# Kernel tuning notes

Measured on AMD Instinct MI355X. Metric: run time of the kernel, lower is better.

## Reference

```python
import jax, jax.numpy as jnp
import numpy as np

_METRIC = (1.0, 1.0, 1.0, 0.0)  # e1,e2,e3 square to +1; e0 (bit 3) squares to 0 (PGA)


def _build_table() -> np.ndarray:
    # Blades ordered by (grade, bits): matches GRADE_INDICES in the source
    # grade1 -> bits 1,2,4,8 at indices 1..4; grade2 -> bits 3,5,6,9,10,12 at 5..10, etc.
    bits_list = sorted(range(16), key=lambda b: (bin(b).count('1'), b))
    idx_of = {b: i for i, b in enumerate(bits_list)}
    table = np.zeros((16, 16, 16), dtype=np.float32)
    for i, bi in enumerate(bits_list):
        for j, bj in enumerate(bits_list):
            swaps = 0
            for k in range(4):
                if (bi >> k) & 1:
                    swaps += bin(bj & ((1 << k) - 1)).count('1')
            coeff = -1.0 if (swaps % 2) else 1.0
            common = bi & bj
            # metric factor: any shared e0 (bit 3) annihilates the term
            if common & 8:
                continue  # metric 0 for e0
            # shared e1/e2/e3 contribute factor +1 (metric +1)
            table[i, j, idx_of[bi ^ bj]] = coeff
    return table


TABLE = jnp.asarray(_build_table())
REV_SIGNS = jnp.asarray(
    [1., 1., 1., 1., 1., -1., -1., -1., -1., -1., -1., -1., -1., -1., -1., 1.],
    dtype=jnp.float32,
)


def geometric_product(a, b):
    # ...i , ...j , ijk -> ...k  (fixed sparse structure-constant contraction)
    return jnp.einsum('...i,...j,ijk->...k', a, b, TABLE.astype(a.dtype))


def setup_inputs() -> dict:
    key = jax.random.key(0)
    kx, km = jax.random.split(key)
    x = jax.random.normal(kx, (16, 262144, 16), dtype=jnp.float32)   # [B, T, 16]
    motor = jax.random.normal(km, (16, 16), dtype=jnp.float32)       # [B, 16]
    return {'x': x, 'motor': motor}


def reference(x, motor):
    # Multivector(x).apply_motor(Multivector(motor)) with 2D motor / 3D data:
    # out = motor * x * reverse(motor), motor broadcast over the token dim.
    signs = REV_SIGNS.astype(motor.dtype)
    m = motor[:, None, :]                # [B, 1, 16] broadcasts over T
    m_rev = (motor * signs)[:, None, :]  # [B, 1, 16]
    tmp = geometric_product(m, x)        # [B, T, 16]
    out = geometric_product(tmp, m_rev)  # [B, T, 16]
    return out
```

## Files before the change

kernel.cpp:

```cpp
#include <hip/hip_runtime.h>

#define PPB 262144
#define NBATCH 16
#define TPB 256
#define NPT 8

typedef float f32x4 __attribute__((ext_vector_type(4)));

static __device__ const int   kBits[16]  = {0,1,2,4,8,3,5,6,9,10,12,7,11,13,14,15};
static __device__ const int   kIdxOf[16] = {0,1,2,5,3,6,7,11,4,8,9,12,10,13,14,15};
static __device__ const float kRev[16]   = {1,1,1,1,1,-1,-1,-1,-1,-1,-1,-1,-1,-1,-1,1};

__global__ void build_sandwich(const float* __restrict__ motor, float* __restrict__ M)
{
    __shared__ float T[16][16][16];
    __shared__ float A[16][16];
    __shared__ float B[16][16];
    __shared__ float m[16], mrev[16];
    const int t = threadIdx.x;
    const int r = t >> 4, c = t & 15;
    const int b = blockIdx.x;

    if (t < 16) { float mv = motor[b * 16 + t]; m[t] = mv; mrev[t] = mv * kRev[t]; }

    #pragma unroll
    for (int k = 0; k < 16; ++k) T[r][c][k] = 0.f;
    {
        const int bi = kBits[r], bj = kBits[c];
        int swaps = 0;
        #pragma unroll
        for (int k = 0; k < 4; ++k)
            if ((bi >> k) & 1) swaps += __popc(bj & ((1 << k) - 1));
        if (!((bi & bj) & 8))
            T[r][c][kIdxOf[bi ^ bj]] = (swaps & 1) ? -1.f : 1.f;
    }
    __syncthreads();

    float av = 0.f, bv = 0.f;
    #pragma unroll
    for (int i = 0; i < 16; ++i) {
        av += m[i]    * T[i][c][r];
        bv += mrev[i] * T[c][i][r];
    }
    A[r][c] = av;
    B[r][c] = bv;
    __syncthreads();

    float acc = 0.f;
    #pragma unroll
    for (int k = 0; k < 16; ++k) acc += B[r][k] * A[k][c];
    M[b * 256 + t] = acc;
}

template<int CTRL>
__device__ inline float dpp1(float v) {
    int i = __float_as_int(v);
    i = __builtin_amdgcn_update_dpp(0, i, CTRL, 0xF, 0xF, true);
    return __int_as_float(i);
}
template<int CTRL>
__device__ inline float4 dpp4(float4 v) {
    float4 r;
    r.x = dpp1<CTRL>(v.x);
    r.y = dpp1<CTRL>(v.y);
    r.z = dpp1<CTRL>(v.z);
    r.w = dpp1<CTRL>(v.w);
    return r;
}

__device__ inline float dot4(float4 a, float4 b) {
    return a.x * b.x + a.y * b.y + a.z * b.z + a.w * b.w;
}

__global__ __launch_bounds__(TPB) void apply_sandwich(
    const f32x4* __restrict__ x, const float* __restrict__ M,
    f32x4* __restrict__ out)
{
    const int t = threadIdx.x;
    const int q = t & 3;
    const int b = blockIdx.y;

    const float* Mb = M + (size_t)b * 256;
    float4 m0_0, m0_1, m0_2, m0_3;
    float4 m1_0, m1_1, m1_2, m1_3;
    float4 m2_0, m2_1, m2_2, m2_3;
    float4 m3_0, m3_1, m3_2, m3_3;
    {
        const int r0 = 4 * q;
        m0_0 = *(const float4*)(Mb + (r0 + 0) * 16 + 4 * (q ^ 0));
        m0_1 = *(const float4*)(Mb + (r0 + 0) * 16 + 4 * (q ^ 1));
        m0_2 = *(const float4*)(Mb + (r0 + 0) * 16 + 4 * (q ^ 2));
        m0_3 = *(const float4*)(Mb + (r0 + 0) * 16 + 4 * (q ^ 3));
        m1_0 = *(const float4*)(Mb + (r0 + 1) * 16 + 4 * (q ^ 0));
        m1_1 = *(const float4*)(Mb + (r0 + 1) * 16 + 4 * (q ^ 1));
        m1_2 = *(const float4*)(Mb + (r0 + 1) * 16 + 4 * (q ^ 2));
        m1_3 = *(const float4*)(Mb + (r0 + 1) * 16 + 4 * (q ^ 3));
        m2_0 = *(const float4*)(Mb + (r0 + 2) * 16 + 4 * (q ^ 0));
        m2_1 = *(const float4*)(Mb + (r0 + 2) * 16 + 4 * (q ^ 1));
        m2_2 = *(const float4*)(Mb + (r0 + 2) * 16 + 4 * (q ^ 2));
        m2_3 = *(const float4*)(Mb + (r0 + 2) * 16 + 4 * (q ^ 3));
        m3_0 = *(const float4*)(Mb + (r0 + 3) * 16 + 4 * (q ^ 0));
        m3_1 = *(const float4*)(Mb + (r0 + 3) * 16 + 4 * (q ^ 1));
        m3_2 = *(const float4*)(Mb + (r0 + 3) * 16 + 4 * (q ^ 2));
        m3_3 = *(const float4*)(Mb + (r0 + 3) * 16 + 4 * (q ^ 3));
    }

    const size_t base = (size_t)b * (PPB * 4) + (size_t)blockIdx.x * (TPB * NPT) + t;

    #pragma unroll
    for (int k = 0; k < NPT; ++k) {
        const size_t g = base + (size_t)k * TPB;
        const f32x4 xv = __builtin_nontemporal_load(&x[g]);
        float4 x0;
        x0.x = xv.x; x0.y = xv.y; x0.z = xv.z; x0.w = xv.w;
        const float4 x1 = dpp4<0xB1>(x0);
        const float4 x2 = dpp4<0x4E>(x0);
        const float4 x3 = dpp4<0x1B>(x0);

        f32x4 acc;
        acc.x = dot4(m0_0, x0) + dot4(m0_1, x1) + dot4(m0_2, x2) + dot4(m0_3, x3);
        acc.y = dot4(m1_0, x0) + dot4(m1_1, x1) + dot4(m1_2, x2) + dot4(m1_3, x3);
        acc.z = dot4(m2_0, x0) + dot4(m2_1, x1) + dot4(m2_2, x2) + dot4(m2_3, x3);
        acc.w = dot4(m3_0, x0) + dot4(m3_1, x1) + dot4(m3_2, x2) + dot4(m3_3, x3);

        __builtin_nontemporal_store(acc, &out[g]);
    }
}

extern "C" void kernel_launch(void* const* d_in, const int* in_sizes, int n_in,
                              void* d_out, int out_size, void* d_ws, size_t ws_size,
                              hipStream_t stream)
{
    const float* x     = (const float*)d_in[0];
    const float* motor = (const float*)d_in[1];
    float* out = (float*)d_out;
    float* M   = (float*)d_ws;

    build_sandwich<<<NBATCH, 256, 0, stream>>>(motor, M);

    dim3 grid(PPB * 4 / (TPB * NPT), NBATCH);
    apply_sandwich<<<grid, TPB, 0, stream>>>((const f32x4*)x, M, (f32x4*)out);
}
```

Before: 96.62 us.

## Fuse sandwich-matrix construction into the apply kernel, dropping the separate launch

Removes the separate build_sandwich kernel and has every block of the main kernel rebuild the 16x16 sandwich matrix for its batch in shared memory. It builds it from the motor with closed-form sign and index lookups packed into 64-bit constants, so no full 16x16x16 structure table is materialised. The intent is to save one kernel launch and the serial dependency between the two kernels. The cost is redundant per-block setup work and three extra barriers before the streaming loop.

```diff
diff --git a/kernel.cpp b/kernel.cpp
--- a/kernel.cpp
+++ b/kernel.cpp
@@ -7,49 +7,19 @@
 
 typedef float f32x4 __attribute__((ext_vector_type(4)));
 
-static __device__ const int   kBits[16]  = {0,1,2,4,8,3,5,6,9,10,12,7,11,13,14,15};
-static __device__ const int   kIdxOf[16] = {0,1,2,5,3,6,7,11,4,8,9,12,10,13,14,15};
-static __device__ const float kRev[16]   = {1,1,1,1,1,-1,-1,-1,-1,-1,-1,-1,-1,-1,-1,1};
+#define PACK_BITS  0xFEDB7CA965384210ull
+#define PACK_IDXOF 0xFEDAC984B7635210ull
+#define REV_NEG_MASK 0x7FE0
 
-__global__ void build_sandwich(const float* __restrict__ motor, float* __restrict__ M)
-{
-    __shared__ float T[16][16][16];
-    __shared__ float A[16][16];
-    __shared__ float B[16][16];
-    __shared__ float m[16], mrev[16];
-    const int t = threadIdx.x;
-    const int r = t >> 4, c = t & 15;
-    const int b = blockIdx.x;
+__device__ __forceinline__ int bits_of(int i) { return (int)((PACK_BITS  >> (4 * i)) & 15ull); }
+__device__ __forceinline__ int idx_of (int b) { return (int)((PACK_IDXOF >> (4 * b)) & 15ull); }
 
-    if (t < 16) { float mv = motor[b * 16 + t]; m[t] = mv; mrev[t] = mv * kRev[t]; }
-
+__device__ __forceinline__ float sign_of(int bl, int br) {
+    int swaps = 0;
     #pragma unroll
-    for (int k = 0; k < 16; ++k) T[r][c][k] = 0.f;
-    {
-        const int bi = kBits[r], bj = kBits[c];
-        int swaps = 0;
-        #pragma unroll
-        for (int k = 0; k < 4; ++k)
-            if ((bi >> k) & 1) swaps += __popc(bj & ((1 << k) - 1));
-        if (!((bi & bj) & 8))
-            T[r][c][kIdxOf[bi ^ bj]] = (swaps & 1) ? -1.f : 1.f;
-    }
-    __syncthreads();
-
-    float av = 0.f, bv = 0.f;
-    #pragma unroll
-    for (int i = 0; i < 16; ++i) {
-        av += m[i]    * T[i][c][r];
-        bv += mrev[i] * T[c][i][r];
-    }
-    A[r][c] = av;
-    B[r][c] = bv;
-    __syncthreads();
-
-    float acc = 0.f;
-    #pragma unroll
-    for (int k = 0; k < 16; ++k) acc += B[r][k] * A[k][c];
-    M[b * 256 + t] = acc;
+    for (int k = 0; k < 4; ++k)
+        if ((bl >> k) & 1) swaps += __popc(br & ((1 << k) - 1));
+    return (swaps & 1) ? -1.f : 1.f;
 }
 
 template<int CTRL>
@@ -72,38 +42,62 @@
     return a.x * b.x + a.y * b.y + a.z * b.z + a.w * b.w;
 }
 
-__global__ __launch_bounds__(TPB) void apply_sandwich(
-    const f32x4* __restrict__ x, const float* __restrict__ M,
+__global__ __launch_bounds__(TPB) void sandwich_fused(
+    const f32x4* __restrict__ x, const float* __restrict__ motor,
     f32x4* __restrict__ out)
 {
+    __shared__ float mS[16], mrevS[16];
+    __shared__ float A[16][16];
+    __shared__ float B[16][16];
+    __shared__ __align__(16) float Ms[16][16];
+
     const int t = threadIdx.x;
     const int q = t & 3;
     const int b = blockIdx.y;
+    const int r = t >> 4, c = t & 15;
 
-    const float* Mb = M + (size_t)b * 256;
-    float4 m0_0, m0_1, m0_2, m0_3;
-    float4 m1_0, m1_1, m1_2, m1_3;
-    float4 m2_0, m2_1, m2_2, m2_3;
-    float4 m3_0, m3_1, m3_2, m3_3;
+    if (t < 16) {
+        float mv = motor[b * 16 + t];
+        mS[t] = mv;
+        mrevS[t] = ((REV_NEG_MASK >> t) & 1) ? -mv : mv;
+    }
+    __syncthreads();
+
     {
-        const int r0 = 4 * q;
-        m0_0 = *(const float4*)(Mb + (r0 + 0) * 16 + 4 * (q ^ 0));
-        m0_1 = *(const float4*)(Mb + (r0 + 0) * 16 + 4 * (q ^ 1));
-        m0_2 = *(const float4*)(Mb + (r0 + 0) * 16 + 4 * (q ^ 2));
-        m0_3 = *(const float4*)(Mb + (r0 + 0) * 16 + 4 * (q ^ 3));
-        m1_0 = *(const float4*)(Mb + (r0 + 1) * 16 + 4 * (q ^ 0));
-        m1_1 = *(const float4*)(Mb + (r0 + 1) * 16 + 4 * (q ^ 1));
-        m1_2 = *(const float4*)(Mb + (r0 + 1) * 16 + 4 * (q ^ 2));
-        m1_3 = *(const float4*)(Mb + (r0 + 1) * 16 + 4 * (q ^ 3));
-        m2_0 = *(const float4*)(Mb + (r0 + 2) * 16 + 4 * (q ^ 0));
-        m2_1 = *(const float4*)(Mb + (r0 + 2) * 16 + 4 * (q ^ 1));
-        m2_2 = *(const float4*)(Mb + (r0 + 2) * 16 + 4 * (q ^ 2));
-        m2_3 = *(const float4*)(Mb + (r0 + 2) * 16 + 4 * (q ^ 3));
-        m3_0 = *(const float4*)(Mb + (r0 + 3) * 16 + 4 * (q ^ 0));
-        m3_1 = *(const float4*)(Mb + (r0 + 3) * 16 + 4 * (q ^ 1));
-        m3_2 = *(const float4*)(Mb + (r0 + 3) * 16 + 4 * (q ^ 2));
-        m3_3 = *(const float4*)(Mb + (r0 + 3) * 16 + 4 * (q ^ 3));
+        const int br = bits_of(r), bc = bits_of(c);
+        const int bx = br ^ bc;
+        const int ii = idx_of(bx);
+        const bool dead = ((bx & bc) & 8) != 0;
+        A[r][c] = dead ? 0.f : sign_of(bx, bc) * mS[ii];
+        B[r][c] = dead ? 0.f : sign_of(bc, bx) * mrevS[ii];
     }
+    __syncthreads();
+
+    {
+        float acc = 0.f;
+        #pragma unroll
+        for (int k = 0; k < 16; ++k) acc += B[r][k] * A[k][c];
+        Ms[r][c] = acc;
+    }
+    __syncthreads();
+
+    const int r0 = 4 * q;
+    const float4 m0_0 = *(const float4*)&Ms[r0 + 0][4 * (q ^ 0)];
+    const float4 m0_1 = *(const float4*)&Ms[r0 + 0][4 * (q ^ 1)];
+    const float4 m0_2 = *(const float4*)&Ms[r0 + 0][4 * (q ^ 2)];
+    const float4 m0_3 = *(const float4*)&Ms[r0 + 0][4 * (q ^ 3)];
+    const float4 m1_0 = *(const float4*)&Ms[r0 + 1][4 * (q ^ 0)];
+    const float4 m1_1 = *(const float4*)&Ms[r0 + 1][4 * (q ^ 1)];
+    const float4 m1_2 = *(const float4*)&Ms[r0 + 1][4 * (q ^ 2)];
+    const float4 m1_3 = *(const float4*)&Ms[r0 + 1][4 * (q ^ 3)];
+    const float4 m2_0 = *(const float4*)&Ms[r0 + 2][4 * (q ^ 0)];
+    const float4 m2_1 = *(const float4*)&Ms[r0 + 2][4 * (q ^ 1)];
+    const float4 m2_2 = *(const float4*)&Ms[r0 + 2][4 * (q ^ 2)];
+    const float4 m2_3 = *(const float4*)&Ms[r0 + 2][4 * (q ^ 3)];
+    const float4 m3_0 = *(const float4*)&Ms[r0 + 3][4 * (q ^ 0)];
+    const float4 m3_1 = *(const float4*)&Ms[r0 + 3][4 * (q ^ 1)];
+    const float4 m3_2 = *(const float4*)&Ms[r0 + 3][4 * (q ^ 2)];
+    const float4 m3_3 = *(const float4*)&Ms[r0 + 3][4 * (q ^ 3)];
 
     const size_t base = (size_t)b * (PPB * 4) + (size_t)blockIdx.x * (TPB * NPT) + t;
 
@@ -134,10 +128,7 @@
     const float* x     = (const float*)d_in[0];
     const float* motor = (const float*)d_in[1];
     float* out = (float*)d_out;
-    float* M   = (float*)d_ws;
-
-    build_sandwich<<<NBATCH, 256, 0, stream>>>(motor, M);
 
     dim3 grid(PPB * 4 / (TPB * NPT), NBATCH);
-    apply_sandwich<<<grid, TPB, 0, stream>>>((const f32x4*)x, M, (f32x4*)out);
+    sandwich_fused<<<grid, TPB, 0, stream>>>((const f32x4*)x, motor, (f32x4*)out);
 }
```

Result: faster. 90.01 us (-6.8%).
